# Kernel optimization log

Hardware: AMD Instinct MI355X
Metric: run time of the kernel (lower is better)

Reference implementation:

```python
import jax, jax.numpy as jnp
import numpy as np

N = 8192      # nodes
D_IN = 128    # input features
D_H = 48      # GAT hidden (hardcoded in module)
D_OUT = 32    # control output dim
NEG_INF = -9e15  # matches torch code's -9000000000000000.0


def setup_inputs() -> dict:
    key = jax.random.key(0)
    ks = jax.random.split(key, 12)
    s = 0.05
    return {
        "x": jax.random.normal(ks[0], (N, D_IN), jnp.float32),
        "adj": jax.random.randint(ks[1], (N, N), 0, 2, jnp.int32),
        "W_gat": jax.random.normal(ks[2], (D_H, D_IN), jnp.float32) * s,
        "a": jax.random.normal(ks[3], (1, D_H), jnp.float32) * s,
        "gamma": jnp.ones((D_H,), jnp.float32),
        "beta": jnp.zeros((D_H,), jnp.float32),
        "W1": jax.random.normal(ks[4], (256, D_H), jnp.float32) * s,
        "b1": jnp.zeros((256,), jnp.float32),
        "W2": jax.random.normal(ks[5], (128, 256), jnp.float32) * s,
        "b2": jnp.zeros((128,), jnp.float32),
        "W3": jax.random.normal(ks[6], (D_OUT, 128), jnp.float32) * s,
        "b3": jnp.zeros((D_OUT,), jnp.float32),
    }


def reference(x, adj, W_gat, a, gamma, beta, W1, b1, W2, b2, W3, b3):
    # --- LightweightGATLayer ---
    Wh = x @ W_gat.T                      # [N, D_H]
    s = Wh @ a.T                          # [N, 1] additive attention scores
    e = s + s.T                           # [N, N]
    e = jnp.where(e > 0, e, 0.2 * e)      # LeakyReLU(0.2)
    e = jnp.where(adj > 0, e, NEG_INF)    # mask non-edges
    attn = jax.nn.softmax(e, axis=1)      # row softmax; dropout is identity in eval
    h_prime = attn @ Wh                   # [N, D_H]
    # LayerNorm over last dim, eps=1e-5
    mu = jnp.mean(h_prime, axis=-1, keepdims=True)
    var = jnp.var(h_prime, axis=-1, keepdims=True)
    h = (h_prime - mu) * jax.lax.rsqrt(var + 1e-5) * gamma + beta
    # --- BiACT MLP head: 48 -> 256 -> 128 -> D_OUT ---
    h = jax.nn.relu(h @ W1.T + b1)
    h = jax.nn.relu(h @ W2.T + b2)
    return h @ W3.T + b3                  # [N, D_OUT]
```

## Files before the change

### kernel.cpp

```cpp
#include <hip/hip_runtime.h>

#define N 8192
#define DIN 128
#define DH 48
#define MT 128
#define KC 64
#define PSTR (KC + 8)
#define NSPLIT 16
#define JSPAN (N / NSPLIT)
#define NCHUNK (JSPAN / KC)
#define ACC_STRIDE 64
#define RB 32

typedef _Float16 half8 __attribute__((ext_vector_type(8)));
typedef float f32x4 __attribute__((ext_vector_type(4)));

__global__ __launch_bounds__(256) void k_wh(const float* __restrict__ x,
                                            const float* __restrict__ Wg,
                                            float* __restrict__ Wh) {
    __shared__ float wT[DIN * DH];
    int t = threadIdx.x;
    for (int e = t; e < DIN * DH; e += 256) {
        int c = e / DIN, k = e % DIN;
        wT[k * DH + c] = Wg[e];
    }
    __syncthreads();
    int o = blockIdx.x * 256 + t;
    int r = o / DH, c = o % DH;
    const float4* xr = (const float4*)(x + (size_t)r * DIN);
    float acc = 0.f;
    #pragma unroll 8
    for (int k4 = 0; k4 < DIN / 4; ++k4) {
        float4 xv = xr[k4];
        int kb = k4 * 4;
        acc += xv.x * wT[(kb + 0) * DH + c];
        acc += xv.y * wT[(kb + 1) * DH + c];
        acc += xv.z * wT[(kb + 2) * DH + c];
        acc += xv.w * wT[(kb + 3) * DH + c];
    }
    Wh[o] = acc;
}

__global__ __launch_bounds__(256) void k_s(const float* __restrict__ Wh,
                                           const float* __restrict__ a,
                                           float* __restrict__ s) {
    int r = blockIdx.x * 256 + threadIdx.x;
    const float4* wr = (const float4*)(Wh + (size_t)r * DH);
    const float4* av = (const float4*)a;
    float acc = 0.f;
    #pragma unroll
    for (int k4 = 0; k4 < DH / 4; ++k4) {
        float4 w = wr[k4]; float4 aa = av[k4];
        acc += w.x * aa.x + w.y * aa.y + w.z * aa.z + w.w * aa.w;
    }
    s[r] = acc;
}

__global__ __launch_bounds__(256) void k_tr(const float* __restrict__ Wh,
                                            _Float16* __restrict__ WhT16) {
    int o = blockIdx.x * 256 + threadIdx.x;
    int d = o >> 13, j = o & 8191;
    _Float16 v;
    if (d < DH)       v = (_Float16)Wh[(size_t)j * DH + d];
    else if (d == DH) v = (_Float16)1.0f;
    else              v = (_Float16)0.0f;
    WhT16[o] = v;
}

__global__ __launch_bounds__(256, 3) void k_gat(const int* __restrict__ adj,
                                                const _Float16* __restrict__ WhT16,
                                                const float* __restrict__ s,
                                                float* __restrict__ accWs) {
    __shared__ _Float16 pS[MT][PSTR];
    __shared__ float sRow[MT];
    int t = threadIdx.x;
    int tile = blockIdx.x & 63;
    int split = blockIdx.x >> 6;
    int i0 = tile * MT;
    int jbase = split * JSPAN;

    int lane = t & 63, w = t >> 6;
    int ln16 = lane & 15, kq = lane >> 4;
    int jp = lane & 31, rh = lane >> 5;

    int rw = w * 32;
    const int* adjBase = adj + (size_t)(i0 + rw + rh * 16) * N + jbase + 2 * jp;

    if (lane < 32) sRow[rw + lane] = s[i0 + rw + lane];

    int2 adjR[16];
    #pragma unroll
    for (int it = 0; it < 16; ++it)
        adjR[it] = *(const int2*)(adjBase + (size_t)it * N);

    f32x4 acc[2][4];
    #pragma unroll
    for (int a0 = 0; a0 < 2; ++a0)
        #pragma unroll
        for (int b0 = 0; b0 < 4; ++b0) acc[a0][b0] = (f32x4){0.f, 0.f, 0.f, 0.f};

    for (int chunk = 0; chunk < NCHUNK; ++chunk) {
        int j0 = jbase + chunk * KC;
        half8 bf[2][4];
        #pragma unroll
        for (int kt = 0; kt < 2; ++kt)
            #pragma unroll
            for (int nt = 0; nt < 4; ++nt)
                bf[kt][nt] = *(const half8*)&WhT16[(size_t)(nt * 16 + ln16) * N
                                                  + j0 + kt * 32 + kq * 8];
        {
            float2 sj = *(const float2*)(s + j0 + 2 * jp);
            #pragma unroll
            for (int it = 0; it < 16; ++it) {
                int r = rw + rh * 16 + it;
                int2 av = adjR[it];
                float e0 = sRow[r] + sj.x;
                float e1 = sRow[r] + sj.y;
                e0 = fmaxf(e0, 0.2f * e0);
                e1 = fmaxf(e1, 0.2f * e1);
                float p0 = av.x ? __expf(e0) : 0.f;
                float p1 = av.y ? __expf(e1) : 0.f;
                union { _Float16 h[2]; unsigned u; } pk;
                pk.h[0] = (_Float16)p0;
                pk.h[1] = (_Float16)p1;
                *(unsigned*)&pS[r][2 * jp] = pk.u;
            }
        }
        if (chunk < NCHUNK - 1) {
            #pragma unroll
            for (int it = 0; it < 16; ++it)
                adjR[it] = *(const int2*)(adjBase + (size_t)it * N + (chunk + 1) * KC);
        }
        #pragma unroll
        for (int kt = 0; kt < 2; ++kt) {
            const int kk = kt * 32 + kq * 8;
            #pragma unroll
            for (int mtl = 0; mtl < 2; ++mtl) {
                half8 a = *(const half8*)&pS[rw + mtl * 16 + ln16][kk];
                #pragma unroll
                for (int nt = 0; nt < 4; ++nt)
                    acc[mtl][nt] = __builtin_amdgcn_mfma_f32_16x16x32_f16(
                        a, bf[kt][nt], acc[mtl][nt], 0, 0, 0);
            }
        }
    }
    size_t rbase = (size_t)split * N + i0;
    #pragma unroll
    for (int mtl = 0; mtl < 2; ++mtl) {
        #pragma unroll
        for (int nt = 0; nt < 4; ++nt) {
            int col = nt * 16 + ln16;
            if (nt == 3 && ln16 != 0) continue;
            #pragma unroll
            for (int reg = 0; reg < 4; ++reg) {
                int row = rw + mtl * 16 + kq * 4 + reg;
                accWs[(rbase + row) * ACC_STRIDE + col] = acc[mtl][nt][reg];
            }
        }
    }
}

__global__ __launch_bounds__(256) void k_mlp(const float* __restrict__ accWs,
                                             const float* __restrict__ gamma,
                                             const float* __restrict__ beta,
                                             const float* __restrict__ W1, const float* __restrict__ b1,
                                             const float* __restrict__ W2, const float* __restrict__ b2,
                                             const float* __restrict__ W3, const float* __restrict__ b3,
                                             float* __restrict__ out) {
    __shared__ float hacc[RB * 49];
    __shared__ _Float16 hN[RB * 72];
    __shared__ _Float16 h1[RB * 264];
    __shared__ float h2[RB * 132];
    int t = threadIdx.x;
    int r0 = blockIdx.x * RB;
    int lane = t & 63, w = t >> 6;
    int ln16 = lane & 15, kq = lane >> 4;

    for (int e = t; e < RB * 49; e += 256) {
        int r = e / 49, d = e % 49;
        size_t base = (size_t)(r0 + r) * ACC_STRIDE + d;
        float v = 0.f;
        #pragma unroll
        for (int sp = 0; sp < NSPLIT; ++sp)
            v += accWs[(size_t)sp * N * ACC_STRIDE + base];
        hacc[e] = v;
    }
    __syncthreads();

    if (t < RB) {
        float invl = 1.f / hacc[t * 49 + 48];
        float sum = 0.f;
        for (int d = 0; d < DH; ++d) sum += hacc[t * 49 + d];
        float mean = sum * invl * (1.f / DH);
        float var = 0.f;
        for (int d = 0; d < DH; ++d) {
            float dv = hacc[t * 49 + d] * invl - mean;
            var += dv * dv;
        }
        var *= (1.f / DH);
        float rs = rsqrtf(var + 1e-5f);
        for (int d = 0; d < DH; ++d) {
            float hv = (hacc[t * 49 + d] * invl - mean) * rs;
            hN[t * 72 + d] = (_Float16)(hv * gamma[d] + beta[d]);
        }
        for (int d = DH; d < 72; ++d) hN[t * 72 + d] = (_Float16)0.f;
    }
    __syncthreads();

    {
        f32x4 acc1[2][4];
        #pragma unroll
        for (int mt = 0; mt < 2; ++mt)
            #pragma unroll
            for (int nt = 0; nt < 4; ++nt) acc1[mt][nt] = (f32x4){0.f, 0.f, 0.f, 0.f};
        #pragma unroll
        for (int kt = 0; kt < 2; ++kt) {
            int k = kt * 32 + kq * 8;
            half8 a[2];
            #pragma unroll
            for (int mt = 0; mt < 2; ++mt)
                a[mt] = *(const half8*)&hN[(mt * 16 + ln16) * 72 + k];
            #pragma unroll
            for (int ntl = 0; ntl < 4; ++ntl) {
                int n = (w * 4 + ntl) * 16 + ln16;
                half8 b;
                #pragma unroll
                for (int i = 0; i < 8; ++i) b[i] = (_Float16)0.f;
                if (k < DH) {
                    float4 lo = *(const float4*)(W1 + n * DH + k);
                    float4 hi = *(const float4*)(W1 + n * DH + k + 4);
                    b[0] = (_Float16)lo.x; b[1] = (_Float16)lo.y;
                    b[2] = (_Float16)lo.z; b[3] = (_Float16)lo.w;
                    b[4] = (_Float16)hi.x; b[5] = (_Float16)hi.y;
                    b[6] = (_Float16)hi.z; b[7] = (_Float16)hi.w;
                }
                #pragma unroll
                for (int mt = 0; mt < 2; ++mt)
                    acc1[mt][ntl] = __builtin_amdgcn_mfma_f32_16x16x32_f16(
                        a[mt], b, acc1[mt][ntl], 0, 0, 0);
            }
        }
        #pragma unroll
        for (int mt = 0; mt < 2; ++mt)
            #pragma unroll
            for (int ntl = 0; ntl < 4; ++ntl) {
                int col = (w * 4 + ntl) * 16 + ln16;
                float bias = b1[col];
                #pragma unroll
                for (int reg = 0; reg < 4; ++reg) {
                    int row = mt * 16 + kq * 4 + reg;
                    float v = acc1[mt][ntl][reg] + bias;
                    h1[row * 264 + col] = (_Float16)fmaxf(v, 0.f);
                }
            }
    }
    __syncthreads();

    {
        f32x4 acc2[2][2];
        #pragma unroll
        for (int mt = 0; mt < 2; ++mt)
            #pragma unroll
            for (int nt = 0; nt < 2; ++nt) acc2[mt][nt] = (f32x4){0.f, 0.f, 0.f, 0.f};
        #pragma unroll
        for (int kt = 0; kt < 8; ++kt) {
            int k = kt * 32 + kq * 8;
            half8 a[2];
            #pragma unroll
            for (int mt = 0; mt < 2; ++mt)
                a[mt] = *(const half8*)&h1[(mt * 16 + ln16) * 264 + k];
            #pragma unroll
            for (int ntl = 0; ntl < 2; ++ntl) {
                int n = (w * 2 + ntl) * 16 + ln16;
                float4 lo = *(const float4*)(W2 + n * 256 + k);
                float4 hi = *(const float4*)(W2 + n * 256 + k + 4);
                half8 b;
                b[0] = (_Float16)lo.x; b[1] = (_Float16)lo.y;
                b[2] = (_Float16)lo.z; b[3] = (_Float16)lo.w;
                b[4] = (_Float16)hi.x; b[5] = (_Float16)hi.y;
                b[6] = (_Float16)hi.z; b[7] = (_Float16)hi.w;
                #pragma unroll
                for (int mt = 0; mt < 2; ++mt)
                    acc2[mt][ntl] = __builtin_amdgcn_mfma_f32_16x16x32_f16(
                        a[mt], b, acc2[mt][ntl], 0, 0, 0);
            }
        }
        #pragma unroll
        for (int mt = 0; mt < 2; ++mt)
            #pragma unroll
            for (int ntl = 0; ntl < 2; ++ntl) {
                int col = (w * 2 + ntl) * 16 + ln16;
                float bias = b2[col];
                #pragma unroll
                for (int reg = 0; reg < 4; ++reg) {
                    int row = mt * 16 + kq * 4 + reg;
                    h2[row * 132 + col] = fmaxf(acc2[mt][ntl][reg] + bias, 0.f);
                }
            }
    }
    __syncthreads();

    {
        int c = t & 31;
        int g = t >> 5;
        int rb = g * 4;
        float acc[4];
        float bias = b3[c];
        #pragma unroll
        for (int r = 0; r < 4; ++r) acc[r] = bias;
        const float4* wrow = (const float4*)(W3 + c * 128);
        for (int k4 = 0; k4 < 32; ++k4) {
            float4 wv = wrow[k4];
            #pragma unroll
            for (int r = 0; r < 4; ++r) {
                const float4 hv = *(const float4*)(&h2[(rb + r) * 132 + k4 * 4]);
                acc[r] += wv.x * hv.x + wv.y * hv.y + wv.z * hv.z + wv.w * hv.w;
            }
        }
        #pragma unroll
        for (int r = 0; r < 4; ++r)
            out[(size_t)(r0 + rb + r) * 32 + c] = acc[r];
    }
}

extern "C" void kernel_launch(void* const* d_in, const int* in_sizes, int n_in,
                              void* d_out, int out_size, void* d_ws, size_t ws_size,
                              hipStream_t stream) {
    const float* x     = (const float*)d_in[0];
    const int*   adj   = (const int*)d_in[1];
    const float* Wg    = (const float*)d_in[2];
    const float* a     = (const float*)d_in[3];
    const float* gamma = (const float*)d_in[4];
    const float* beta  = (const float*)d_in[5];
    const float* W1    = (const float*)d_in[6];
    const float* b1    = (const float*)d_in[7];
    const float* W2    = (const float*)d_in[8];
    const float* b2    = (const float*)d_in[9];
    const float* W3    = (const float*)d_in[10];
    const float* b3    = (const float*)d_in[11];
    float* out = (float*)d_out;

    float* ws = (float*)d_ws;
    float* Wh       = ws;
    float* s        = ws + (size_t)N * DH;
    _Float16* WhT16 = (_Float16*)(s + N);
    float* accWs    = (float*)((char*)WhT16 + (size_t)64 * N * sizeof(_Float16));

    k_wh<<<N * DH / 256, 256, 0, stream>>>(x, Wg, Wh);
    k_s<<<N / 256, 256, 0, stream>>>(Wh, a, s);
    k_tr<<<64 * N / 256, 256, 0, stream>>>(Wh, WhT16);
    k_gat<<<64 * NSPLIT, 256, 0, stream>>>(adj, WhT16, s, accWs);
    k_mlp<<<N / RB, 256, 0, stream>>>(accWs, gamma, beta, W1, b1, W2, b2, W3, b3, out);
}
```

Measured before the change: 456.3 us.

## Restructure GAT tile: each wave owns 16 rows, full-span LDS with swizzle

The GAT kernel now uses 64-row tiles across 2048 blocks, and each wave handles 16 rows. A wave computes the exp-weighted masked scores for its whole 512-column span up front with 16-byte adjacency loads, and writes them to a 64x512 fp16 LDS buffer using an XOR swizzle to avoid bank conflicts. It then runs the MFMA loop without any per-chunk barriers. This removes the interleaved chunk pipeline and issues wider, more coalesced adj reads, but it uses more LDS (64 KB), which lowers occupancy to 2 blocks per CU, and each block reloads the WhT16 B fragments for only 16 rows per wave, so reuse drops.

```diff
diff --git a/kernel.cpp b/kernel.cpp
--- a/kernel.cpp
+++ b/kernel.cpp
@@ -3,12 +3,9 @@
 #define N 8192
 #define DIN 128
 #define DH 48
-#define MT 128
-#define KC 64
-#define PSTR (KC + 8)
 #define NSPLIT 16
-#define JSPAN (N / NSPLIT)
-#define NCHUNK (JSPAN / KC)
+#define SPAN (N / NSPLIT)
+#define MTK 64
 #define ACC_STRIDE 64
 #define RB 32
 
@@ -67,40 +64,67 @@
     WhT16[o] = v;
 }
 
-__global__ __launch_bounds__(256, 3) void k_gat(const int* __restrict__ adj,
+__global__ __launch_bounds__(256, 2) void k_gat(const int* __restrict__ adj,
                                                 const _Float16* __restrict__ WhT16,
                                                 const float* __restrict__ s,
                                                 float* __restrict__ accWs) {
-    __shared__ _Float16 pS[MT][PSTR];
-    __shared__ float sRow[MT];
+    __shared__ _Float16 pS[MTK][SPAN];
     int t = threadIdx.x;
-    int tile = blockIdx.x & 63;
-    int split = blockIdx.x >> 6;
-    int i0 = tile * MT;
-    int jbase = split * JSPAN;
+    int tile = blockIdx.x & 127;
+    int split = blockIdx.x >> 7;
+    int i0 = tile * MTK;
+    int jbase = split * SPAN;
 
     int lane = t & 63, w = t >> 6;
     int ln16 = lane & 15, kq = lane >> 4;
-    int jp = lane & 31, rh = lane >> 5;
-
-    int rw = w * 32;
-    const int* adjBase = adj + (size_t)(i0 + rw + rh * 16) * N + jbase + 2 * jp;
-
-    if (lane < 32) sRow[rw + lane] = s[i0 + rw + lane];
-
-    int2 adjR[16];
-    #pragma unroll
-    for (int it = 0; it < 16; ++it)
-        adjR[it] = *(const int2*)(adjBase + (size_t)it * N);
-
-    f32x4 acc[2][4];
-    #pragma unroll
-    for (int a0 = 0; a0 < 2; ++a0)
-        #pragma unroll
-        for (int b0 = 0; b0 < 4; ++b0) acc[a0][b0] = (f32x4){0.f, 0.f, 0.f, 0.f};
-
-    for (int chunk = 0; chunk < NCHUNK; ++chunk) {
-        int j0 = jbase + chunk * KC;
+    int rw = w * 16;
+
+    float srw[16];
+    #pragma unroll
+    for (int k = 0; k < 16; ++k) srw[k] = s[i0 + rw + k];
+    float4 sj0 = *(const float4*)(s + jbase + 4 * lane);
+    float4 sj1 = *(const float4*)(s + jbase + 256 + 4 * lane);
+
+    const int* adjW = adj + (size_t)(i0 + rw) * N + jbase;
+    #pragma unroll
+    for (int r = 0; r < 16; ++r) {
+        int4 a0 = *(const int4*)(adjW + (size_t)r * N + 4 * lane);
+        int4 a1 = *(const int4*)(adjW + (size_t)r * N + 256 + 4 * lane);
+        float sr = srw[r];
+        union { _Float16 h[4]; double d; } pk0, pk1;
+        {
+            float e0 = sr + sj0.x, e1 = sr + sj0.y, e2 = sr + sj0.z, e3 = sr + sj0.w;
+            e0 = fmaxf(e0, 0.2f * e0); e1 = fmaxf(e1, 0.2f * e1);
+            e2 = fmaxf(e2, 0.2f * e2); e3 = fmaxf(e3, 0.2f * e3);
+            pk0.h[0] = (_Float16)(a0.x ? __expf(e0) : 0.f);
+            pk0.h[1] = (_Float16)(a0.y ? __expf(e1) : 0.f);
+            pk0.h[2] = (_Float16)(a0.z ? __expf(e2) : 0.f);
+            pk0.h[3] = (_Float16)(a0.w ? __expf(e3) : 0.f);
+        }
+        {
+            float e0 = sr + sj1.x, e1 = sr + sj1.y, e2 = sr + sj1.z, e3 = sr + sj1.w;
+            e0 = fmaxf(e0, 0.2f * e0); e1 = fmaxf(e1, 0.2f * e1);
+            e2 = fmaxf(e2, 0.2f * e2); e3 = fmaxf(e3, 0.2f * e3);
+            pk1.h[0] = (_Float16)(a1.x ? __expf(e0) : 0.f);
+            pk1.h[1] = (_Float16)(a1.y ? __expf(e1) : 0.f);
+            pk1.h[2] = (_Float16)(a1.z ? __expf(e2) : 0.f);
+            pk1.h[3] = (_Float16)(a1.w ? __expf(e3) : 0.f);
+        }
+        char* rowp = (char*)&pS[rw + r][0];
+        int swz = (r & 7) << 4;
+        *(double*)(rowp + ((8 * lane) ^ swz)) = pk0.d;
+        *(double*)(rowp + (512 + ((8 * lane) ^ swz))) = pk1.d;
+    }
+
+    f32x4 acc[4];
+    #pragma unroll
+    for (int nt = 0; nt < 4; ++nt) acc[nt] = (f32x4){0.f, 0.f, 0.f, 0.f};
+
+    const char* arp = (const char*)&pS[rw + ln16][0];
+    const int aswz = (ln16 & 7) << 4;
+    #pragma unroll
+    for (int c = 0; c < 8; ++c) {
+        int j0 = jbase + c * 64;
         half8 bf[2][4];
         #pragma unroll
         for (int kt = 0; kt < 2; ++kt)
@@ -108,54 +132,25 @@
             for (int nt = 0; nt < 4; ++nt)
                 bf[kt][nt] = *(const half8*)&WhT16[(size_t)(nt * 16 + ln16) * N
                                                   + j0 + kt * 32 + kq * 8];
-        {
-            float2 sj = *(const float2*)(s + j0 + 2 * jp);
-            #pragma unroll
-            for (int it = 0; it < 16; ++it) {
-                int r = rw + rh * 16 + it;
-                int2 av = adjR[it];
-                float e0 = sRow[r] + sj.x;
-                float e1 = sRow[r] + sj.y;
-                e0 = fmaxf(e0, 0.2f * e0);
-                e1 = fmaxf(e1, 0.2f * e1);
-                float p0 = av.x ? __expf(e0) : 0.f;
-                float p1 = av.y ? __expf(e1) : 0.f;
-                union { _Float16 h[2]; unsigned u; } pk;
-                pk.h[0] = (_Float16)p0;
-                pk.h[1] = (_Float16)p1;
-                *(unsigned*)&pS[r][2 * jp] = pk.u;
-            }
-        }
-        if (chunk < NCHUNK - 1) {
-            #pragma unroll
-            for (int it = 0; it < 16; ++it)
-                adjR[it] = *(const int2*)(adjBase + (size_t)it * N + (chunk + 1) * KC);
-        }
         #pragma unroll
         for (int kt = 0; kt < 2; ++kt) {
-            const int kk = kt * 32 + kq * 8;
-            #pragma unroll
-            for (int mtl = 0; mtl < 2; ++mtl) {
-                half8 a = *(const half8*)&pS[rw + mtl * 16 + ln16][kk];
-                #pragma unroll
-                for (int nt = 0; nt < 4; ++nt)
-                    acc[mtl][nt] = __builtin_amdgcn_mfma_f32_16x16x32_f16(
-                        a, bf[kt][nt], acc[mtl][nt], 0, 0, 0);
-            }
-        }
-    }
-    size_t rbase = (size_t)split * N + i0;
-    #pragma unroll
-    for (int mtl = 0; mtl < 2; ++mtl) {
-        #pragma unroll
-        for (int nt = 0; nt < 4; ++nt) {
-            int col = nt * 16 + ln16;
-            if (nt == 3 && ln16 != 0) continue;
-            #pragma unroll
-            for (int reg = 0; reg < 4; ++reg) {
-                int row = rw + mtl * 16 + kq * 4 + reg;
-                accWs[(rbase + row) * ACC_STRIDE + col] = acc[mtl][nt][reg];
-            }
+            half8 a = *(const half8*)(arp + ((c * 128 + kt * 64 + kq * 16) ^ aswz));
+            #pragma unroll
+            for (int nt = 0; nt < 4; ++nt)
+                acc[nt] = __builtin_amdgcn_mfma_f32_16x16x32_f16(
+                    a, bf[kt][nt], acc[nt], 0, 0, 0);
+        }
+    }
+
+    size_t rbase = (size_t)split * N + i0 + rw;
+    #pragma unroll
+    for (int nt = 0; nt < 4; ++nt) {
+        int col = nt * 16 + ln16;
+        if (nt == 3 && ln16 != 0) continue;
+        #pragma unroll
+        for (int reg = 0; reg < 4; ++reg) {
+            int row = kq * 4 + reg;
+            accWs[(rbase + row) * ACC_STRIDE + col] = acc[nt][reg];
         }
     }
 }
@@ -349,6 +344,6 @@
     k_wh<<<N * DH / 256, 256, 0, stream>>>(x, Wg, Wh);
     k_s<<<N / 256, 256, 0, stream>>>(Wh, a, s);
     k_tr<<<64 * N / 256, 256, 0, stream>>>(Wh, WhT16);
-    k_gat<<<64 * NSPLIT, 256, 0, stream>>>(adj, WhT16, s, accWs);
+    k_gat<<<128 * NSPLIT, 256, 0, stream>>>(adj, WhT16, s, accWs);
     k_mlp<<<N / RB, 256, 0, stream>>>(accWs, gamma, beta, W1, b1, W2, b2, W3, b3, out);
 }
```

New measurement: 472.5 us. 1.04x slower.

## Pack adjacency into bitmask and build MFMA A-fragments in registers

Applied to the files above, without the earlier changes.

A new pre-pass packs the int32 adjacency matrix into 64-bit bitmasks. The GAT kernel then reads the bitmask and computes the exp attention values directly into MFMA A-fragment registers, so the shared-memory staging of P and its barrier-free LDS round trip go away. It also raises the occupancy hint to 4 and sets wave priority around the MFMA block. The full 256MB adjacency is still read once by the pack kernel, so the main saving is removing LDS traffic and the per-lane register prefetch of adjacency. The cost is redundant exp work: the same sj values are recomputed per row-fragment, plus an extra launch and mask buffer.

```diff
diff --git a/kernel.cpp b/kernel.cpp
--- a/kernel.cpp
+++ b/kernel.cpp
@@ -3,12 +3,10 @@
 #define N 8192
 #define DIN 128
 #define DH 48
-#define MT 128
-#define KC 64
-#define PSTR (KC + 8)
 #define NSPLIT 16
-#define JSPAN (N / NSPLIT)
-#define NCHUNK (JSPAN / KC)
+#define SPAN (N / NSPLIT)
+#define NCHUNK (SPAN / 64)
+#define NW64 (N / 64)
 #define ACC_STRIDE 64
 #define RB 32
 
@@ -67,31 +65,58 @@
     WhT16[o] = v;
 }
 
-__global__ __launch_bounds__(256, 3) void k_gat(const int* __restrict__ adj,
+__global__ __launch_bounds__(256) void k_pack(const int* __restrict__ adj,
+                                              unsigned long long* __restrict__ mask) {
+    size_t o = (size_t)blockIdx.x * 256 + threadIdx.x;
+    const int4* p = (const int4*)(adj + o * 64);
+    unsigned long long m = 0;
+    #pragma unroll
+    for (int g = 0; g < 16; ++g) {
+        int4 a = p[g];
+        m |= ((unsigned long long)(a.x != 0)) << (4 * g + 0);
+        m |= ((unsigned long long)(a.y != 0)) << (4 * g + 1);
+        m |= ((unsigned long long)(a.z != 0)) << (4 * g + 2);
+        m |= ((unsigned long long)(a.w != 0)) << (4 * g + 3);
+    }
+    mask[o] = m;
+}
+
+__device__ __forceinline__ half8 mk_afrag(float si, const float* __restrict__ sjp,
+                                          unsigned b8) {
+    float4 lo = *(const float4*)sjp;
+    float4 hi = *(const float4*)(sjp + 4);
+    half8 a;
+    float e;
+    e = si + lo.x; e = fmaxf(e, 0.2f * e); a[0] = (_Float16)((b8 & 1u)   ? __expf(e) : 0.f);
+    e = si + lo.y; e = fmaxf(e, 0.2f * e); a[1] = (_Float16)((b8 & 2u)   ? __expf(e) : 0.f);
+    e = si + lo.z; e = fmaxf(e, 0.2f * e); a[2] = (_Float16)((b8 & 4u)   ? __expf(e) : 0.f);
+    e = si + lo.w; e = fmaxf(e, 0.2f * e); a[3] = (_Float16)((b8 & 8u)   ? __expf(e) : 0.f);
+    e = si + hi.x; e = fmaxf(e, 0.2f * e); a[4] = (_Float16)((b8 & 16u)  ? __expf(e) : 0.f);
+    e = si + hi.y; e = fmaxf(e, 0.2f * e); a[5] = (_Float16)((b8 & 32u)  ? __expf(e) : 0.f);
+    e = si + hi.z; e = fmaxf(e, 0.2f * e); a[6] = (_Float16)((b8 & 64u)  ? __expf(e) : 0.f);
+    e = si + hi.w; e = fmaxf(e, 0.2f * e); a[7] = (_Float16)((b8 & 128u) ? __expf(e) : 0.f);
+    return a;
+}
+
+__global__ __launch_bounds__(256, 4) void k_gat(const unsigned long long* __restrict__ mask,
                                                 const _Float16* __restrict__ WhT16,
                                                 const float* __restrict__ s,
                                                 float* __restrict__ accWs) {
-    __shared__ _Float16 pS[MT][PSTR];
-    __shared__ float sRow[MT];
     int t = threadIdx.x;
     int tile = blockIdx.x & 63;
     int split = blockIdx.x >> 6;
-    int i0 = tile * MT;
-    int jbase = split * JSPAN;
+    int i0 = tile * 128;
+    int jbase = split * SPAN;
 
     int lane = t & 63, w = t >> 6;
     int ln16 = lane & 15, kq = lane >> 4;
-    int jp = lane & 31, rh = lane >> 5;
-
     int rw = w * 32;
-    const int* adjBase = adj + (size_t)(i0 + rw + rh * 16) * N + jbase + 2 * jp;
-
-    if (lane < 32) sRow[rw + lane] = s[i0 + rw + lane];
-
-    int2 adjR[16];
-    #pragma unroll
-    for (int it = 0; it < 16; ++it)
-        adjR[it] = *(const int2*)(adjBase + (size_t)it * N);
+
+    float si0 = s[i0 + rw + ln16];
+    float si1 = s[i0 + rw + 16 + ln16];
+    const unsigned long long* mrow0 =
+        mask + (size_t)(i0 + rw + ln16) * NW64 + split * NCHUNK;
+    const unsigned long long* mrow1 = mrow0 + (size_t)16 * NW64;
 
     f32x4 acc[2][4];
     #pragma unroll
@@ -99,8 +124,19 @@
         #pragma unroll
         for (int b0 = 0; b0 < 4; ++b0) acc[a0][b0] = (f32x4){0.f, 0.f, 0.f, 0.f};
 
-    for (int chunk = 0; chunk < NCHUNK; ++chunk) {
-        int j0 = jbase + chunk * KC;
+    #pragma unroll 2
+    for (int c = 0; c < NCHUNK; ++c) {
+        int j0 = jbase + c * 64;
+        unsigned long long m0 = mrow0[c];
+        unsigned long long m1 = mrow1[c];
+        half8 af[2][2];
+        #pragma unroll
+        for (int kt = 0; kt < 2; ++kt) {
+            const float* sjp = s + j0 + kt * 32 + kq * 8;
+            int sh = kt * 32 + kq * 8;
+            af[0][kt] = mk_afrag(si0, sjp, (unsigned)(m0 >> sh) & 0xffu);
+            af[1][kt] = mk_afrag(si1, sjp, (unsigned)(m1 >> sh) & 0xffu);
+        }
         half8 bf[2][4];
         #pragma unroll
         for (int kt = 0; kt < 2; ++kt)
@@ -108,42 +144,18 @@
             for (int nt = 0; nt < 4; ++nt)
                 bf[kt][nt] = *(const half8*)&WhT16[(size_t)(nt * 16 + ln16) * N
                                                   + j0 + kt * 32 + kq * 8];
-        {
-            float2 sj = *(const float2*)(s + j0 + 2 * jp);
-            #pragma unroll
-            for (int it = 0; it < 16; ++it) {
-                int r = rw + rh * 16 + it;
-                int2 av = adjR[it];
-                float e0 = sRow[r] + sj.x;
-                float e1 = sRow[r] + sj.y;
-                e0 = fmaxf(e0, 0.2f * e0);
-                e1 = fmaxf(e1, 0.2f * e1);
-                float p0 = av.x ? __expf(e0) : 0.f;
-                float p1 = av.y ? __expf(e1) : 0.f;
-                union { _Float16 h[2]; unsigned u; } pk;
-                pk.h[0] = (_Float16)p0;
-                pk.h[1] = (_Float16)p1;
-                *(unsigned*)&pS[r][2 * jp] = pk.u;
-            }
-        }
-        if (chunk < NCHUNK - 1) {
-            #pragma unroll
-            for (int it = 0; it < 16; ++it)
-                adjR[it] = *(const int2*)(adjBase + (size_t)it * N + (chunk + 1) * KC);
-        }
-        #pragma unroll
-        for (int kt = 0; kt < 2; ++kt) {
-            const int kk = kt * 32 + kq * 8;
-            #pragma unroll
-            for (int mtl = 0; mtl < 2; ++mtl) {
-                half8 a = *(const half8*)&pS[rw + mtl * 16 + ln16][kk];
+        __builtin_amdgcn_s_setprio(1);
+        #pragma unroll
+        for (int kt = 0; kt < 2; ++kt)
+            #pragma unroll
+            for (int mtl = 0; mtl < 2; ++mtl)
                 #pragma unroll
                 for (int nt = 0; nt < 4; ++nt)
                     acc[mtl][nt] = __builtin_amdgcn_mfma_f32_16x16x32_f16(
-                        a, bf[kt][nt], acc[mtl][nt], 0, 0, 0);
-            }
-        }
-    }
+                        af[mtl][kt], bf[kt][nt], acc[mtl][nt], 0, 0, 0);
+        __builtin_amdgcn_s_setprio(0);
+    }
+
     size_t rbase = (size_t)split * N + i0;
     #pragma unroll
     for (int mtl = 0; mtl < 2; ++mtl) {
@@ -340,15 +352,18 @@
     const float* b3    = (const float*)d_in[11];
     float* out = (float*)d_out;
 
-    float* ws = (float*)d_ws;
-    float* Wh       = ws;
-    float* s        = ws + (size_t)N * DH;
-    _Float16* WhT16 = (_Float16*)(s + N);
-    float* accWs    = (float*)((char*)WhT16 + (size_t)64 * N * sizeof(_Float16));
-
+    char* ws = (char*)d_ws;
+    float* Wh       = (float*)ws;
+    float* s        = (float*)(ws + (size_t)N * DH * 4);
+    _Float16* WhT16 = (_Float16*)(ws + (size_t)N * DH * 4 + N * 4);
+    float* accWs    = (float*)((char*)WhT16 + (size_t)64 * N * 2);
+    unsigned long long* mask64 =
+        (unsigned long long*)((char*)accWs + (size_t)NSPLIT * N * ACC_STRIDE * 4);
+
+    k_pack<<<N * (N / 64) / 256, 256, 0, stream>>>(adj, mask64);
     k_wh<<<N * DH / 256, 256, 0, stream>>>(x, Wg, Wh);
     k_s<<<N / 256, 256, 0, stream>>>(Wh, a, s);
     k_tr<<<64 * N / 256, 256, 0, stream>>>(Wh, WhT16);
-    k_gat<<<64 * NSPLIT, 256, 0, stream>>>(adj, WhT16, s, accWs);
+    k_gat<<<64 * NSPLIT, 256, 0, stream>>>(mask64, WhT16, s, accWs);
     k_mlp<<<N / RB, 256, 0, stream>>>(accWs, gamma, beta, W1, b1, W2, b2, W3, b3, out);
 }
```

Result: slower. 467.4 us (+2.4%).
